# Kernel tuning notes

Measured on AMD Instinct MI355X. Metric: run time of the kernel, lower is better.

Reference implementation:

```python
import jax, jax.numpy as jnp
import numpy as np

B, C, H, W = 8, 256, 160, 160
CRED, GROUPS = 64, 8
EPS = 1e-4      # curvature eps (module arg)
GN_EPS = 1e-5   # torch GroupNorm default


def _depthwise3x3(y, k33):
    # y: [B,Cr,H,W]; k33: [3,3] fixed kernel applied per-channel
    k = jnp.broadcast_to(k33, (CRED, 1, 3, 3)).astype(y.dtype)
    return jax.lax.conv_general_dilated(
        y, k, window_strides=(1, 1), padding='SAME',
        feature_group_count=CRED,
        dimension_numbers=('NCHW', 'OIHW', 'NCHW'))


def setup_inputs() -> dict:
    key = jax.random.key(0)
    ks = jax.random.split(key, 6)
    return {
        'x': jax.random.normal(ks[0], (B, C, H, W), jnp.float32),
        'reduce_w': jax.random.normal(ks[1], (CRED, C, 1, 1), jnp.float32) * 0.05,
        'gn_scale': jnp.ones((CRED,), jnp.float32),
        'gn_bias': jnp.zeros((CRED,), jnp.float32),
        'gate_w1': jax.random.normal(ks[2], (16, CRED, 1, 1), jnp.float32) * 0.1,
        'gate_b1': jnp.zeros((16,), jnp.float32),
        'gate_w2': jax.random.normal(ks[3], (CRED, 16, 1, 1), jnp.float32) * 0.1,
        'gate_b2': jnp.zeros((CRED,), jnp.float32),
        'fuse_w': jax.random.normal(ks[4], (1, 2 * CRED, 1, 1), jnp.float32) * 0.1,
    }


def reference(x, reduce_w, gn_scale, gn_bias, gate_w1, gate_b1, gate_w2, gate_b2, fuse_w):
    b = x.shape[0]
    # 1x1 reduce conv (no bias)
    y = jnp.einsum('bchw,oc->bohw', x, reduce_w[:, :, 0, 0])
    # GroupNorm(8, 64)
    yg = y.reshape(b, GROUPS, CRED // GROUPS, H, W)
    mean = yg.mean(axis=(2, 3, 4), keepdims=True)
    var = yg.var(axis=(2, 3, 4), keepdims=True)
    y = ((yg - mean) * jax.lax.rsqrt(var + GN_EPS)).reshape(b, CRED, H, W)
    y = y * gn_scale[None, :, None, None] + gn_bias[None, :, None, None]
    # fixed depthwise convs: mean3, sobel-x, sobel-y
    mean_k = jnp.full((3, 3), 1.0 / 9.0, jnp.float32)
    sobel_x = jnp.array([[1., 0., -1.], [2., 0., -2.], [1., 0., -1.]], jnp.float32) / 4.0
    mu = _depthwise3x3(y, mean_k)
    gx = _depthwise3x3(y, sobel_x)
    gy = _depthwise3x3(y, sobel_x.T)
    # curvature elementwise chain
    ratio = jnp.clip(jnp.abs(y - mu) / (jnp.abs(gx) + jnp.abs(gy) + EPS), 0.0, 2.0)
    kappa = jnp.clip(1.0 - ratio, -1.0, 1.0)
    # SE-style gate on y: GAP -> 1x1 -> relu -> 1x1 -> sigmoid
    p = y.mean(axis=(2, 3))                                   # [B,Cr]
    hdn = jax.nn.relu(p @ gate_w1[:, :, 0, 0].T + gate_b1)    # [B,16]
    gamma = jax.nn.sigmoid(hdn @ gate_w2[:, :, 0, 0].T + gate_b2)  # [B,Cr]
    gated = gamma[:, :, None, None] * kappa
    # fuse: 1x1 conv over cat([kappa, gated]) -> sigmoid -> scale 0.1
    fw = fuse_w[0, :, 0, 0]
    a = jax.nn.sigmoid(jnp.einsum('bchw,c->bhw', kappa, fw[:CRED]) +
                       jnp.einsum('bchw,c->bhw', gated, fw[CRED:]))[:, None]
    return x * (1.0 + 0.1 * a)
```

## Files before the change

kernel.cpp:

```cpp
#include <hip/hip_runtime.h>
#include <hip/hip_bf16.h>
#include <math.h>

#define HW2D 25600
#define NB 8
#define NC 256
#define CR 64
#define H_ 160
#define W_ 160

typedef short bf16x8 __attribute__((ext_vector_type(8)));
typedef float f32x4 __attribute__((ext_vector_type(4)));

__device__ __forceinline__ short f2bf(float f) {
    __hip_bfloat16 h = __float2bfloat16(f);
    return *reinterpret_cast<short*>(&h);
}
__device__ __forceinline__ float bf2f(unsigned short b) {
    union { unsigned u; float f; } v; v.u = ((unsigned)b) << 16;
    return v.f;
}

__global__ __launch_bounds__(256) void k_pack(const float* __restrict__ rw,
                                              short* __restrict__ aPack) {
    int t = blockIdx.x * 256 + threadIdx.x;
    if (t >= 2048) return;
    int s = t >> 8, m = (t >> 6) & 3, lane = t & 63;
    int row = m * 16 + (lane & 15);
    int k0 = s * 32 + (lane >> 4) * 8;
    short* dst = aPack + ((size_t)((s * 4 + m) * 64 + lane)) * 8;
#pragma unroll
    for (int j = 0; j < 8; ++j)
        dst[j] = f2bf(rw[row * NC + k0 + j]);
}

__global__ __launch_bounds__(256) void k_rmfma(const float* __restrict__ x,
                                               const short* __restrict__ aPack,
                                               unsigned short* __restrict__ y1,
                                               float* __restrict__ part) {
    int wave = __builtin_amdgcn_readfirstlane(threadIdx.x >> 6);
    int lane = threadIdx.x & 63;
    int blk = blockIdx.x;
    int b = blk / 200;
    int pxb = (blk - b * 200) * 128 + wave * 32;
    int l15 = lane & 15, kg = lane >> 4;
    int laneoff = kg * 8 * HW2D + l15;
    const float* xw = x + (size_t)b * NC * HW2D + pxb;
    f32x4 acc[4][2];
    f32x4 zz = {0.f, 0.f, 0.f, 0.f};
#pragma unroll
    for (int m = 0; m < 4; ++m)
#pragma unroll
        for (int n = 0; n < 2; ++n) acc[m][n] = zz;
    const bf16x8* ap = (const bf16x8*)aPack + lane;
#pragma unroll
    for (int s = 0; s < 8; ++s) {
        bf16x8 a0 = ap[(s * 4 + 0) * 64];
        bf16x8 a1 = ap[(s * 4 + 1) * 64];
        bf16x8 a2 = ap[(s * 4 + 2) * 64];
        bf16x8 a3 = ap[(s * 4 + 3) * 64];
        const float* xs = xw + s * 32 * HW2D + laneoff;
        bf16x8 b0, b1;
#pragma unroll
        for (int j = 0; j < 8; ++j) {
            b0[j] = f2bf(xs[j * HW2D]);
            b1[j] = f2bf(xs[j * HW2D + 16]);
        }
        acc[0][0] = __builtin_amdgcn_mfma_f32_16x16x32_bf16(a0, b0, acc[0][0], 0, 0, 0);
        acc[0][1] = __builtin_amdgcn_mfma_f32_16x16x32_bf16(a0, b1, acc[0][1], 0, 0, 0);
        acc[1][0] = __builtin_amdgcn_mfma_f32_16x16x32_bf16(a1, b0, acc[1][0], 0, 0, 0);
        acc[1][1] = __builtin_amdgcn_mfma_f32_16x16x32_bf16(a1, b1, acc[1][1], 0, 0, 0);
        acc[2][0] = __builtin_amdgcn_mfma_f32_16x16x32_bf16(a2, b0, acc[2][0], 0, 0, 0);
        acc[2][1] = __builtin_amdgcn_mfma_f32_16x16x32_bf16(a2, b1, acc[2][1], 0, 0, 0);
        acc[3][0] = __builtin_amdgcn_mfma_f32_16x16x32_bf16(a3, b0, acc[3][0], 0, 0, 0);
        acc[3][1] = __builtin_amdgcn_mfma_f32_16x16x32_bf16(a3, b1, acc[3][1], 0, 0, 0);
    }
    __shared__ unsigned short tr[4][32 * 66];
    __shared__ float st_s[4][64], st_q[4][64];
    unsigned short* trw = tr[wave];
#pragma unroll
    for (int m = 0; m < 4; ++m)
#pragma unroll
        for (int n = 0; n < 2; ++n)
#pragma unroll
            for (int i = 0; i < 4; i += 2) {
                unsigned short r0 = (unsigned short)f2bf(acc[m][n][i]);
                unsigned short r1 = (unsigned short)f2bf(acc[m][n][i + 1]);
                unsigned v = (unsigned)r0 | ((unsigned)r1 << 16);
                int o = m * 16 + kg * 4 + i;
                *(unsigned*)&trw[(n * 16 + l15) * 66 + o] = v;
            }
    float cs[8], cq[8];
#pragma unroll
    for (int k = 0; k < 8; ++k) { cs[k] = 0.f; cq[k] = 0.f; }
    unsigned short* yg = y1 + ((size_t)b * HW2D + pxb) * 64;
    const int e = lane & 7, a = lane >> 3;
#pragma unroll
    for (int j = 0; j < 4; ++j) {
        int p = j * 8 + a;
        int dbase = p * 66 + e * 8;
        unsigned q0 = *(const unsigned*)&trw[dbase];
        unsigned q1 = *(const unsigned*)&trw[dbase + 2];
        unsigned q2 = *(const unsigned*)&trw[dbase + 4];
        unsigned q3 = *(const unsigned*)&trw[dbase + 6];
        uint4 vv; vv.x = q0; vv.y = q1; vv.z = q2; vv.w = q3;
        *(uint4*)(yg + (size_t)p * 64 + e * 8) = vv;
        float f0 = bf2f((unsigned short)(q0 & 0xffff)), f1 = bf2f((unsigned short)(q0 >> 16));
        float f2 = bf2f((unsigned short)(q1 & 0xffff)), f3 = bf2f((unsigned short)(q1 >> 16));
        float f4 = bf2f((unsigned short)(q2 & 0xffff)), f5 = bf2f((unsigned short)(q2 >> 16));
        float f6 = bf2f((unsigned short)(q3 & 0xffff)), f7 = bf2f((unsigned short)(q3 >> 16));
        cs[0] += f0; cq[0] = fmaf(f0, f0, cq[0]);
        cs[1] += f1; cq[1] = fmaf(f1, f1, cq[1]);
        cs[2] += f2; cq[2] = fmaf(f2, f2, cq[2]);
        cs[3] += f3; cq[3] = fmaf(f3, f3, cq[3]);
        cs[4] += f4; cq[4] = fmaf(f4, f4, cq[4]);
        cs[5] += f5; cq[5] = fmaf(f5, f5, cq[5]);
        cs[6] += f6; cq[6] = fmaf(f6, f6, cq[6]);
        cs[7] += f7; cq[7] = fmaf(f7, f7, cq[7]);
    }
#pragma unroll
    for (int k = 0; k < 8; ++k) {
#pragma unroll
        for (int off = 8; off < 64; off <<= 1) {
            cs[k] += __shfl_xor(cs[k], off, 64);
            cq[k] += __shfl_xor(cq[k], off, 64);
        }
    }
    if (a == 0) {
#pragma unroll
        for (int k = 0; k < 8; ++k) {
            st_s[wave][e * 8 + k] = cs[k];
            st_q[wave][e * 8 + k] = cq[k];
        }
    }
    __syncthreads();
    int tt = threadIdx.x;
    if (tt < 64)
        part[(size_t)blk * 128 + tt] = st_s[0][tt] + st_s[1][tt] + st_s[2][tt] + st_s[3][tt];
    else if (tt < 128)
        part[(size_t)blk * 128 + tt] =
            st_q[0][tt - 64] + st_q[1][tt - 64] + st_q[2][tt - 64] + st_q[3][tt - 64];
}

__global__ __launch_bounds__(512) void k_gate(const float* __restrict__ part,
                                              const float* __restrict__ gn_scale,
                                              const float* __restrict__ gn_bias,
                                              const float* __restrict__ w1,
                                              const float* __restrict__ b1,
                                              const float* __restrict__ w2,
                                              const float* __restrict__ b2,
                                              const float* __restrict__ fw,
                                              float* __restrict__ sA,
                                              float* __restrict__ sB,
                                              float* __restrict__ wef) {
    int t = threadIdx.x;
    int b = t >> 6, c = t & 63;
    __shared__ float sh_sum[512], sh_sq[512], sh_p[512], sh_h[128];
    float s = 0.f, sq = 0.f;
    const float* pb = part + (size_t)b * 200 * 128;
    for (int k = 0; k < 200; ++k) {
        s  += pb[k * 128 + c];
        sq += pb[k * 128 + 64 + c];
    }
    sh_sum[t] = s;
    sh_sq[t] = sq;
    __syncthreads();
    int base = (t & ~7);
    float gs = 0.f, gq = 0.f;
#pragma unroll
    for (int i = 0; i < 8; ++i) { gs += sh_sum[base + i]; gq += sh_sq[base + i]; }
    const float invN = 1.0f / (8.0f * HW2D);
    float mean = gs * invN;
    float var = gq * invN - mean * mean;
    float rstd = rsqrtf(var + 1e-5f);
    float A = rstd * gn_scale[c];
    float Bv = gn_bias[c] - mean * A;
    sA[t] = A;
    sB[t] = Bv;
    float chmean = s * (1.0f / HW2D);
    sh_p[t] = chmean * A + Bv;
    __syncthreads();
    if (t < 128) {
        int bb = t >> 4, j = t & 15;
        float h = b1[j];
        for (int i = 0; i < 64; ++i) h = fmaf(sh_p[bb * 64 + i], w1[j * 64 + i], h);
        sh_h[t] = fmaxf(h, 0.f);
    }
    __syncthreads();
    float gacc = b2[c];
#pragma unroll
    for (int j = 0; j < 16; ++j) gacc = fmaf(sh_h[b * 16 + j], w2[c * 16 + j], gacc);
    float gamma = 1.0f / (1.0f + expf(-gacc));
    wef[t] = fw[c] + gamma * fw[CR + c];
}

__global__ __launch_bounds__(256) void k_sten(const unsigned short* __restrict__ y1,
                                              const float* __restrict__ sA,
                                              const float* __restrict__ sB,
                                              const float* __restrict__ wef,
                                              float* __restrict__ abuf) {
    const int tw = blockIdx.x * 16, th = blockIdx.y * 4, b = blockIdx.z;
    __shared__ unsigned short hal[108 * 66];
    __shared__ float sh_part[4][64];
    const int t = threadIdx.x;
    const int w = __builtin_amdgcn_readfirstlane(t >> 6);
    const int lane = t & 63;
    const unsigned short* yb = y1 + (size_t)b * HW2D * 64;

#pragma unroll
    for (int it = 0; it < 4; ++it) {
        int i = t + it * 256;
        if (i < 864) {
            int pxi = i >> 3, c8 = (i & 7) * 8;
            int r = pxi / 18, u = pxi - r * 18;
            int gh = th + r - 1, gw = tw + u - 1;
            uint4 v; v.x = 0u; v.y = 0u; v.z = 0u; v.w = 0u;
            if ((unsigned)gh < 160u && (unsigned)gw < 160u)
                v = *(const uint4*)(yb + ((size_t)(gh * W_ + gw)) * 64 + c8);
            int d = pxi * 66 + c8;
            *(unsigned*)&hal[d]     = v.x;
            *(unsigned*)&hal[d + 2] = v.y;
            *(unsigned*)&hal[d + 4] = v.z;
            *(unsigned*)&hal[d + 6] = v.w;
        }
    }
    __syncthreads();

    const int col = lane & 15, prow = lane >> 4;
    const int gh = th + prow, gw = tw + col;
    const int top = (gh == 0), bot = (gh == 159), lef = (gw == 0), rig = (gw == 159);
    const float n9  = (float)(3 * (top + bot) + 3 * (lef + rig) -
                              (top + bot) * (lef + rig)) * (1.f / 9.f);
    const float sOx = (float)(lef - rig) * (float)(4 - top - bot) * 0.25f;
    const float sOy = (float)(top - bot) * (float)(4 - lef - rig) * 0.25f;
    const int p0 = prow * 18 + col;
    const int bc = b * 64;
    const int c0 = w * 16;
    float logit = 0.f;
#pragma unroll
    for (int cp = 0; cp < 8; ++cp) {
        int c = c0 + cp * 2;
        unsigned u00 = *(const unsigned*)&hal[(p0     ) * 66 + c];
        unsigned u01 = *(const unsigned*)&hal[(p0 +  1) * 66 + c];
        unsigned u02 = *(const unsigned*)&hal[(p0 +  2) * 66 + c];
        unsigned u10 = *(const unsigned*)&hal[(p0 + 18) * 66 + c];
        unsigned u11 = *(const unsigned*)&hal[(p0 + 19) * 66 + c];
        unsigned u12 = *(const unsigned*)&hal[(p0 + 20) * 66 + c];
        unsigned u20 = *(const unsigned*)&hal[(p0 + 36) * 66 + c];
        unsigned u21 = *(const unsigned*)&hal[(p0 + 37) * 66 + c];
        unsigned u22 = *(const unsigned*)&hal[(p0 + 38) * 66 + c];
        float A0 = sA[bc + c],     B0 = sB[bc + c],     wf0 = wef[bc + c];
        float A1 = sA[bc + c + 1], B1 = sB[bc + c + 1], wf1 = wef[bc + c + 1];
        {
            float v00 = bf2f((unsigned short)u00), v01 = bf2f((unsigned short)u01);
            float v02 = bf2f((unsigned short)u02), v10 = bf2f((unsigned short)u10);
            float v11 = bf2f((unsigned short)u11), v12 = bf2f((unsigned short)u12);
            float v20 = bf2f((unsigned short)u20), v21 = bf2f((unsigned short)u21);
            float v22 = bf2f((unsigned short)u22);
            float S = (v00 + v01 + v02) + (v10 + v11 + v12) + (v20 + v21 + v22);
            float gxr = (v00 - v02 + 2.f * (v10 - v12) + v20 - v22) * 0.25f;
            float gyr = (v00 - v20 + 2.f * (v01 - v21) + v02 - v22) * 0.25f;
            float dev = fmaf(A0, v11 - S * (1.f / 9.f), B0 * n9);
            float gx  = fmaf(A0, gxr, -B0 * sOx);
            float gy  = fmaf(A0, gyr, -B0 * sOy);
            float ratio = fminf(fabsf(dev) / (fabsf(gx) + fabsf(gy) + 1e-4f), 2.f);
            logit = fmaf(wf0, 1.f - ratio, logit);
        }
        {
            float v00 = bf2f((unsigned short)(u00 >> 16)), v01 = bf2f((unsigned short)(u01 >> 16));
            float v02 = bf2f((unsigned short)(u02 >> 16)), v10 = bf2f((unsigned short)(u10 >> 16));
            float v11 = bf2f((unsigned short)(u11 >> 16)), v12 = bf2f((unsigned short)(u12 >> 16));
            float v20 = bf2f((unsigned short)(u20 >> 16)), v21 = bf2f((unsigned short)(u21 >> 16));
            float v22 = bf2f((unsigned short)(u22 >> 16));
            float S = (v00 + v01 + v02) + (v10 + v11 + v12) + (v20 + v21 + v22);
            float gxr = (v00 - v02 + 2.f * (v10 - v12) + v20 - v22) * 0.25f;
            float gyr = (v00 - v20 + 2.f * (v01 - v21) + v02 - v22) * 0.25f;
            float dev = fmaf(A1, v11 - S * (1.f / 9.f), B1 * n9);
            float gx  = fmaf(A1, gxr, -B1 * sOx);
            float gy  = fmaf(A1, gyr, -B1 * sOy);
            float ratio = fminf(fabsf(dev) / (fabsf(gx) + fabsf(gy) + 1e-4f), 2.f);
            logit = fmaf(wf1, 1.f - ratio, logit);
        }
    }
    sh_part[w][lane] = logit;
    __syncthreads();
    if (t < 64) {
        float l = sh_part[0][t] + sh_part[1][t] + sh_part[2][t] + sh_part[3][t];
        float av = fmaf(0.1f, 1.f / (1.f + expf(-l)), 1.f);
        abuf[(size_t)b * HW2D + (th + (t >> 4)) * W_ + tw + (t & 15)] = av;
    }
}

__global__ __launch_bounds__(256) void k_apply(const float* __restrict__ x,
                                               const float* __restrict__ abuf,
                                               float* __restrict__ out) {
    int px4 = blockIdx.x * 256 + threadIdx.x;
    int c = blockIdx.y, b = blockIdx.z;
    size_t xi = ((size_t)(b * NC + c)) * (HW2D / 4) + px4;
    float4 xv = ((const float4*)x)[xi];
    float4 av = ((const float4*)abuf)[b * (HW2D / 4) + px4];
    float4 ov;
    ov.x = xv.x * av.x;
    ov.y = xv.y * av.y;
    ov.z = xv.z * av.z;
    ov.w = xv.w * av.w;
    ((float4*)out)[xi] = ov;
}

extern "C" void kernel_launch(void* const* d_in, const int* in_sizes, int n_in,
                              void* d_out, int out_size, void* d_ws, size_t ws_size,
                              hipStream_t stream) {
    const float* x   = (const float*)d_in[0];
    const float* rw  = (const float*)d_in[1];
    const float* gns = (const float*)d_in[2];
    const float* gnb = (const float*)d_in[3];
    const float* w1  = (const float*)d_in[4];
    const float* b1  = (const float*)d_in[5];
    const float* w2  = (const float*)d_in[6];
    const float* b2  = (const float*)d_in[7];
    const float* fw  = (const float*)d_in[8];
    float* out = (float*)d_out;

    float* ws    = (float*)d_ws;
    float* sA    = ws;
    float* sB    = sA + 512;
    float* wef   = sB + 512;
    float* part  = wef + 512;
    float* abuf  = part + 204800;
    short* aPack = (short*)(abuf + 204800);
    unsigned short* y1 = (unsigned short*)(aPack + 16384);

    hipLaunchKernelGGL(k_pack,  dim3(8),           dim3(256), 0, stream, rw, aPack);
    hipLaunchKernelGGL(k_rmfma, dim3(1600),        dim3(256), 0, stream, x, aPack, y1, part);
    hipLaunchKernelGGL(k_gate,  dim3(1),           dim3(512), 0, stream,
                       part, gns, gnb, w1, b1, w2, b2, fw, sA, sB, wef);
    hipLaunchKernelGGL(k_sten,  dim3(10, 40, 8),   dim3(256), 0, stream, y1, sA, sB, wef, abuf);
    hipLaunchKernelGGL(k_apply, dim3(25, 256, 8),  dim3(256), 0, stream, x, abuf, out);
}
```

Baseline: 161.6 us.

## Fuse stencil and apply kernels; parallelize gate kernel across batch blocks

The stencil kernel now multiplies x by the attention factor directly for its 16x4 pixel tile across all 256 channels, so the separate apply kernel and the abuf round trip are gone. The gate kernel is split into 8 blocks of 128 threads, one per batch, instead of a single 512-thread block. The fused kernel saves a launch and the abuf write and read, but its x accesses are only 64-byte row segments per channel, which may coalesce worse than the old fully contiguous apply kernel.

```diff
diff --git a/kernel.cpp b/kernel.cpp
--- a/kernel.cpp
+++ b/kernel.cpp
@@ -142,66 +142,66 @@
             st_q[0][tt - 64] + st_q[1][tt - 64] + st_q[2][tt - 64] + st_q[3][tt - 64];
 }
 
-__global__ __launch_bounds__(512) void k_gate(const float* __restrict__ part,
-                                              const float* __restrict__ gn_scale,
-                                              const float* __restrict__ gn_bias,
-                                              const float* __restrict__ w1,
-                                              const float* __restrict__ b1,
-                                              const float* __restrict__ w2,
-                                              const float* __restrict__ b2,
-                                              const float* __restrict__ fw,
-                                              float* __restrict__ sA,
-                                              float* __restrict__ sB,
-                                              float* __restrict__ wef) {
-    int t = threadIdx.x;
-    int b = t >> 6, c = t & 63;
-    __shared__ float sh_sum[512], sh_sq[512], sh_p[512], sh_h[128];
-    float s = 0.f, sq = 0.f;
-    const float* pb = part + (size_t)b * 200 * 128;
-    for (int k = 0; k < 200; ++k) {
-        s  += pb[k * 128 + c];
-        sq += pb[k * 128 + 64 + c];
-    }
-    sh_sum[t] = s;
-    sh_sq[t] = sq;
-    __syncthreads();
-    int base = (t & ~7);
-    float gs = 0.f, gq = 0.f;
-#pragma unroll
-    for (int i = 0; i < 8; ++i) { gs += sh_sum[base + i]; gq += sh_sq[base + i]; }
-    const float invN = 1.0f / (8.0f * HW2D);
-    float mean = gs * invN;
-    float var = gq * invN - mean * mean;
-    float rstd = rsqrtf(var + 1e-5f);
-    float A = rstd * gn_scale[c];
-    float Bv = gn_bias[c] - mean * A;
-    sA[t] = A;
-    sB[t] = Bv;
-    float chmean = s * (1.0f / HW2D);
-    sh_p[t] = chmean * A + Bv;
-    __syncthreads();
-    if (t < 128) {
-        int bb = t >> 4, j = t & 15;
-        float h = b1[j];
-        for (int i = 0; i < 64; ++i) h = fmaf(sh_p[bb * 64 + i], w1[j * 64 + i], h);
+__global__ __launch_bounds__(128) void k_gateB(const float* __restrict__ part,
+                                               const float* __restrict__ gn_scale,
+                                               const float* __restrict__ gn_bias,
+                                               const float* __restrict__ w1,
+                                               const float* __restrict__ b1,
+                                               const float* __restrict__ w2,
+                                               const float* __restrict__ b2,
+                                               const float* __restrict__ fw,
+                                               float* __restrict__ sA,
+                                               float* __restrict__ sB,
+                                               float* __restrict__ wef) {
+    const int b = blockIdx.x, t = threadIdx.x;
+    __shared__ float sh_s[64], sh_q[64], sh_p[64], sh_h[16];
+    const float* pb = part + (size_t)b * 200 * 128 + t;
+    float s = 0.f;
+#pragma unroll 4
+    for (int k = 0; k < 200; ++k) s += pb[(size_t)k * 128];
+    if (t < 64) sh_s[t] = s; else sh_q[t - 64] = s;
+    __syncthreads();
+    if (t < 64) {
+        int c = t, g = c & ~7;
+        float gs = 0.f, gq = 0.f;
+#pragma unroll
+        for (int i = 0; i < 8; ++i) { gs += sh_s[g + i]; gq += sh_q[g + i]; }
+        const float invN = 1.0f / (8.0f * HW2D);
+        float mean = gs * invN;
+        float var = gq * invN - mean * mean;
+        float rstd = rsqrtf(var + 1e-5f);
+        float A = rstd * gn_scale[c];
+        float Bv = gn_bias[c] - mean * A;
+        sA[b * 64 + c] = A;
+        sB[b * 64 + c] = Bv;
+        sh_p[c] = fmaf(sh_s[c] * (1.0f / HW2D), A, Bv);
+    }
+    __syncthreads();
+    if (t < 16) {
+        float h = b1[t];
+        for (int i = 0; i < 64; ++i) h = fmaf(sh_p[i], w1[t * 64 + i], h);
         sh_h[t] = fmaxf(h, 0.f);
     }
     __syncthreads();
-    float gacc = b2[c];
-#pragma unroll
-    for (int j = 0; j < 16; ++j) gacc = fmaf(sh_h[b * 16 + j], w2[c * 16 + j], gacc);
-    float gamma = 1.0f / (1.0f + expf(-gacc));
-    wef[t] = fw[c] + gamma * fw[CR + c];
-}
-
-__global__ __launch_bounds__(256) void k_sten(const unsigned short* __restrict__ y1,
-                                              const float* __restrict__ sA,
-                                              const float* __restrict__ sB,
-                                              const float* __restrict__ wef,
-                                              float* __restrict__ abuf) {
+    if (t < 64) {
+        float g = b2[t];
+#pragma unroll
+        for (int j = 0; j < 16; ++j) g = fmaf(sh_h[j], w2[t * 16 + j], g);
+        float gamma = 1.0f / (1.0f + expf(-g));
+        wef[b * 64 + t] = fw[t] + gamma * fw[CR + t];
+    }
+}
+
+__global__ __launch_bounds__(256) void k_tail2(const unsigned short* __restrict__ y1,
+                                               const float* __restrict__ x,
+                                               const float* __restrict__ sA,
+                                               const float* __restrict__ sB,
+                                               const float* __restrict__ wef,
+                                               float* __restrict__ out) {
     const int tw = blockIdx.x * 16, th = blockIdx.y * 4, b = blockIdx.z;
     __shared__ unsigned short hal[108 * 66];
     __shared__ float sh_part[4][64];
+    __shared__ float sh_av[64];
     const int t = threadIdx.x;
     const int w = __builtin_amdgcn_readfirstlane(t >> 6);
     const int lane = t & 63;
@@ -286,25 +286,26 @@
     __syncthreads();
     if (t < 64) {
         float l = sh_part[0][t] + sh_part[1][t] + sh_part[2][t] + sh_part[3][t];
-        float av = fmaf(0.1f, 1.f / (1.f + expf(-l)), 1.f);
-        abuf[(size_t)b * HW2D + (th + (t >> 4)) * W_ + tw + (t & 15)] = av;
-    }
-}
-
-__global__ __launch_bounds__(256) void k_apply(const float* __restrict__ x,
-                                               const float* __restrict__ abuf,
-                                               float* __restrict__ out) {
-    int px4 = blockIdx.x * 256 + threadIdx.x;
-    int c = blockIdx.y, b = blockIdx.z;
-    size_t xi = ((size_t)(b * NC + c)) * (HW2D / 4) + px4;
-    float4 xv = ((const float4*)x)[xi];
-    float4 av = ((const float4*)abuf)[b * (HW2D / 4) + px4];
-    float4 ov;
-    ov.x = xv.x * av.x;
-    ov.y = xv.y * av.y;
-    ov.z = xv.z * av.z;
-    ov.w = xv.w * av.w;
-    ((float4*)out)[xi] = ov;
+        sh_av[t] = fmaf(0.1f, 1.f / (1.f + expf(-l)), 1.f);
+    }
+    __syncthreads();
+
+    const int slot = t & 15, chb = t >> 4;
+    const int row = slot >> 2, cg4 = slot & 3;
+    float4 a4 = *(const float4*)&sh_av[row * 16 + cg4 * 4];
+    const size_t pbase = ((size_t)(b * NC + chb)) * HW2D
+                       + (size_t)(th + row) * W_ + tw + cg4 * 4;
+#pragma unroll 4
+    for (int i = 0; i < 16; ++i) {
+        size_t xi = pbase + (size_t)i * 16 * HW2D;
+        float4 xv = *(const float4*)(x + xi);
+        float4 ov;
+        ov.x = xv.x * a4.x;
+        ov.y = xv.y * a4.y;
+        ov.z = xv.z * a4.z;
+        ov.w = xv.w * a4.w;
+        *(float4*)(out + xi) = ov;
+    }
 }
 
 extern "C" void kernel_launch(void* const* d_in, const int* in_sizes, int n_in,
@@ -326,14 +327,13 @@
     float* sB    = sA + 512;
     float* wef   = sB + 512;
     float* part  = wef + 512;
-    float* abuf  = part + 204800;
-    short* aPack = (short*)(abuf + 204800);
+    short* aPack = (short*)(part + 204800);
     unsigned short* y1 = (unsigned short*)(aPack + 16384);
 
-    hipLaunchKernelGGL(k_pack,  dim3(8),           dim3(256), 0, stream, rw, aPack);
-    hipLaunchKernelGGL(k_rmfma, dim3(1600),        dim3(256), 0, stream, x, aPack, y1, part);
-    hipLaunchKernelGGL(k_gate,  dim3(1),           dim3(512), 0, stream,
+    hipLaunchKernelGGL(k_pack,  dim3(8),          dim3(256), 0, stream, rw, aPack);
+    hipLaunchKernelGGL(k_rmfma, dim3(1600),       dim3(256), 0, stream, x, aPack, y1, part);
+    hipLaunchKernelGGL(k_gateB, dim3(8),          dim3(128), 0, stream,
                        part, gns, gnb, w1, b1, w2, b2, fw, sA, sB, wef);
-    hipLaunchKernelGGL(k_sten,  dim3(10, 40, 8),   dim3(256), 0, stream, y1, sA, sB, wef, abuf);
-    hipLaunchKernelGGL(k_apply, dim3(25, 256, 8),  dim3(256), 0, stream, x, abuf, out);
-}
+    hipLaunchKernelGGL(k_tail2, dim3(10, 40, 8),  dim3(256), 0, stream,
+                       y1, x, sA, sB, wef, out);
+}
```

Result: slower. 239.2 us (+48.0%).
